# Kernel optimization log

Measured on AMD Instinct MI355X. Metric: run time of the kernel, lower is better.

## Reference

```python
import jax, jax.numpy as jnp
import numpy as np

N_NODES = 100000


def gcn_conv(x, edge_index, W, b, num_nodes):
    """PyG-style GCNConv: add self-loops, symmetric deg normalization,
    linear transform, scatter-add aggregation, bias."""
    src, dst = edge_index[0], edge_index[1]
    loop = jnp.arange(num_nodes, dtype=src.dtype)
    src = jnp.concatenate([src, loop])
    dst = jnp.concatenate([dst, loop])
    # degree (in-degree incl. self loops) and D^{-1/2}
    deg = jax.ops.segment_sum(jnp.ones_like(dst, dtype=x.dtype), dst,
                              num_segments=num_nodes)
    dinv = jnp.where(deg > 0, jax.lax.rsqrt(deg), 0.0)
    norm = dinv[src] * dinv[dst]                       # [E + N]
    h = x @ W                                          # [N, out]
    msg = h[src] * norm[:, None]                       # gather + scale
    out = jax.ops.segment_sum(msg, dst, num_segments=num_nodes)
    return out + b


def setup_inputs() -> dict:
    key = jax.random.key(0)
    ks = jax.random.split(key, 8)
    num_inputs, hidden, num_outputs = 128, 128, 2
    x = jax.random.normal(ks[0], (N_NODES, num_inputs), dtype=jnp.float32)
    edge_index = jax.random.randint(ks[1], (2, 3200000), 0, N_NODES,
                                    dtype=jnp.int64)
    s = 1.0 / np.sqrt(num_inputs)
    W1 = jax.random.uniform(ks[2], (num_inputs, hidden), jnp.float32, -s, s)
    b1 = jnp.zeros((hidden,), jnp.float32)
    s2 = 1.0 / np.sqrt(hidden)
    W2 = jax.random.uniform(ks[3], (hidden, hidden), jnp.float32, -s2, s2)
    b2 = jnp.zeros((hidden,), jnp.float32)
    Wl = jax.random.uniform(ks[4], (hidden, num_outputs), jnp.float32, -s2, s2)
    bl = jax.random.uniform(ks[5], (num_outputs,), jnp.float32, -s2, s2)
    return {"x": x, "edge_index": edge_index, "W1": W1, "b1": b1,
            "W2": W2, "b2": b2, "Wl": Wl, "bl": bl}


def reference(x, edge_index, W1, b1, W2, b2, Wl, bl):
    # eval mode: dropout is identity
    h = gcn_conv(x, edge_index, W1, b1, N_NODES)
    h = jax.nn.relu(h)
    h = gcn_conv(h, edge_index, W2, b2, N_NODES)
    h = jax.nn.relu(h)
    return h @ Wl + bl
```

## Files before the change

### kernel.cpp

```cpp
#include <hip/hip_runtime.h>
#include <hip/hip_bf16.h>


#define NB_T   256
#define NBUCK  256
#define BSHIFT 9
#define EPB    4096

__device__ __forceinline__ unsigned short f2bf(float f) {
    unsigned u = __float_as_uint(f);
    u += 0x7FFF + ((u >> 16) & 1);
    return (unsigned short)(u >> 16);
}
__device__ __forceinline__ float bflo(unsigned u) {
    return __uint_as_float(u << 16);
}
__device__ __forceinline__ float bfhi(unsigned u) {
    return __uint_as_float(u & 0xffff0000u);
}

__global__ void k_zero_buckets(int* bucketTotal) {
    bucketTotal[threadIdx.x] = 0;
}

__global__ __launch_bounds__(NB_T) void k_binCount(const int* __restrict__ src,
                                                   const int* __restrict__ dst,
                                                   int E, int n, int* bucketTotal) {
    __shared__ int hist[NBUCK];
    int t = threadIdx.x;
    hist[t] = 0;
    __syncthreads();
    int lo = blockIdx.x * EPB;
    int hi = min(lo + EPB, E + n);
    for (int e = lo + t; e < hi; e += NB_T) {
        int d = (e < E) ? dst[e] : (e - E);
        atomicAdd(&hist[d >> BSHIFT], 1);
    }
    __syncthreads();
    int h = hist[t];
    if (h) atomicAdd(&bucketTotal[t], h);
}

__global__ void k_bscan(const int* __restrict__ bucketTotal, int* bucketBase,
                        int* bucketCursor, int* rowStart, int E, int n) {
    __shared__ int sh[NBUCK];
    int t = threadIdx.x;
    int v = bucketTotal[t];
    sh[t] = v; __syncthreads();
    for (int off = 1; off < NBUCK; off <<= 1) {
        int u = (t >= off) ? sh[t - off] : 0;
        __syncthreads();
        sh[t] += u;
        __syncthreads();
    }
    int ex = sh[t] - v;
    bucketBase[t] = ex;
    bucketCursor[t] = ex;
    if (t == NBUCK - 1) { bucketBase[NBUCK] = sh[t]; rowStart[n] = E + n; }
}

__global__ __launch_bounds__(NB_T) void k_binScatter(const int* __restrict__ src,
                                                     const int* __restrict__ dst,
                                                     int E, int n, int* bucketCursor,
                                                     unsigned int* __restrict__ binned) {
    __shared__ int hist[NBUCK];
    __shared__ int base[NBUCK];
    int t = threadIdx.x;
    hist[t] = 0;
    __syncthreads();
    int lo = blockIdx.x * EPB;
    int hi = min(lo + EPB, E + n);
    for (int e = lo + t; e < hi; e += NB_T) {
        int d = (e < E) ? dst[e] : (e - E);
        atomicAdd(&hist[d >> BSHIFT], 1);
    }
    __syncthreads();
    int h = hist[t];
    if (h) base[t] = atomicAdd(&bucketCursor[t], h);
    hist[t] = 0;
    __syncthreads();
    for (int e = lo + t; e < hi; e += NB_T) {
        int s, d;
        if (e < E) { s = src[e]; d = dst[e]; }
        else       { s = d = e - E; }
        int b = d >> BSHIFT;
        int pos = base[b] + atomicAdd(&hist[b], 1);
        binned[pos] = ((unsigned)(d & 511) << 17) | (unsigned)s;
    }
}

__global__ __launch_bounds__(NB_T) void k_csr(const unsigned int* __restrict__ binned,
                                              const int* __restrict__ bucketBase,
                                              int* __restrict__ rowStart,
                                              float* __restrict__ dinv,
                                              int* __restrict__ sortedSrc, int n) {
    __shared__ int cnt[512];
    __shared__ int start[512];
    __shared__ int sh[NB_T];
    int b = blockIdx.x, t = threadIdx.x;
    int ebase = bucketBase[b], eend = bucketBase[b + 1];
    cnt[t] = 0; cnt[t + 256] = 0;
    __syncthreads();
    for (int e = ebase + t; e < eend; e += NB_T)
        atomicAdd(&cnt[binned[e] >> 17], 1);
    __syncthreads();
    int c0 = cnt[t * 2], c1 = cnt[t * 2 + 1];
    int ts = c0 + c1;
    sh[t] = ts; __syncthreads();
    for (int off = 1; off < NB_T; off <<= 1) {
        int u = (t >= off) ? sh[t - off] : 0;
        __syncthreads();
        sh[t] += u;
        __syncthreads();
    }
    int pref = sh[t] - ts;
    start[t * 2]     = pref;
    start[t * 2 + 1] = pref + c0;
    __syncthreads();
    int node0 = b << BSHIFT;
    for (int i = t; i < 512; i += NB_T) {
        int node = node0 + i;
        if (node < n) {
            rowStart[node] = ebase + start[i];
            dinv[node] = rsqrtf((float)cnt[i]);
        }
    }
    __syncthreads();
    cnt[t] = 0; cnt[t + 256] = 0;
    __syncthreads();
    for (int e = ebase + t; e < eend; e += NB_T) {
        unsigned p = binned[e];
        int i = p >> 17;
        int pos = ebase + start[i] + atomicAdd(&cnt[i], 1);
        sortedSrc[pos] = (int)(p & 0x1FFFF);
    }
}

__global__ __launch_bounds__(NB_T) void k_cvt(const float* __restrict__ x,
                                              const float* __restrict__ dinv,
                                              unsigned short* __restrict__ xh, int n) {
    int i = blockIdx.x * NB_T + threadIdx.x;
    if (i >= n * 32) return;
    float w = dinv[i >> 5];
    float4 v = *(const float4*)(x + (size_t)i * 4);
    ushort4 o;
    o.x = f2bf(v.x * w); o.y = f2bf(v.y * w);
    o.z = f2bf(v.z * w); o.w = f2bf(v.w * w);
    *(ushort4*)(xh + (size_t)i * 4) = o;
}

__global__ __launch_bounds__(256) void k_agg(const unsigned short* __restrict__ F,
                                             unsigned short* __restrict__ G,
                                             const int* __restrict__ rowStart,
                                             const int* __restrict__ sortedSrc,
                                             const float* __restrict__ dinv, int n) {
    int wave = threadIdx.x >> 6;
    int lane = threadIdx.x & 63;
    int node = blockIdx.x * 4 + wave;
    if (node >= n) return;
    int r0 = rowStart[node], r1 = rowStart[node + 1];
    int half = lane >> 5;
    int c    = lane & 31;
    size_t fo = (size_t)(c * 4);
    float a0 = 0.f, a1 = 0.f, a2 = 0.f, a3 = 0.f;
    int e = r0;
    for (; e + 8 <= r1; e += 8) {
        int s0 = sortedSrc[e     + half];
        int s1 = sortedSrc[e + 2 + half];
        int s2 = sortedSrc[e + 4 + half];
        int s3 = sortedSrc[e + 6 + half];
        uint2 v0 = *(const uint2*)(F + (size_t)s0 * 128 + fo);
        uint2 v1 = *(const uint2*)(F + (size_t)s1 * 128 + fo);
        uint2 v2 = *(const uint2*)(F + (size_t)s2 * 128 + fo);
        uint2 v3 = *(const uint2*)(F + (size_t)s3 * 128 + fo);
        a0 += bflo(v0.x) + bflo(v1.x) + bflo(v2.x) + bflo(v3.x);
        a1 += bfhi(v0.x) + bfhi(v1.x) + bfhi(v2.x) + bfhi(v3.x);
        a2 += bflo(v0.y) + bflo(v1.y) + bflo(v2.y) + bflo(v3.y);
        a3 += bfhi(v0.y) + bfhi(v1.y) + bfhi(v2.y) + bfhi(v3.y);
    }
    for (; e + 2 <= r1; e += 2) {
        int s0 = sortedSrc[e + half];
        uint2 v0 = *(const uint2*)(F + (size_t)s0 * 128 + fo);
        a0 += bflo(v0.x); a1 += bfhi(v0.x);
        a2 += bflo(v0.y); a3 += bfhi(v0.y);
    }
    if (e < r1 && half == 0) {
        int s0 = sortedSrc[e];
        uint2 v0 = *(const uint2*)(F + (size_t)s0 * 128 + fo);
        a0 += bflo(v0.x); a1 += bfhi(v0.x);
        a2 += bflo(v0.y); a3 += bfhi(v0.y);
    }
    a0 += __shfl_xor(a0, 32, 64);
    a1 += __shfl_xor(a1, 32, 64);
    a2 += __shfl_xor(a2, 32, 64);
    a3 += __shfl_xor(a3, 32, 64);
    if (half == 0) {
        float wd = dinv[node];
        ushort4 o;
        o.x = f2bf(a0 * wd); o.y = f2bf(a1 * wd);
        o.z = f2bf(a2 * wd); o.w = f2bf(a3 * wd);
        *(ushort4*)(G + (size_t)node * 128 + fo) = o;
    }
}

__device__ __forceinline__ float f4c(const float4 v, int k) {
    return k == 0 ? v.x : k == 1 ? v.y : k == 2 ? v.z : v.w;
}

template <bool BF16OUT>
__global__ __launch_bounds__(256, 4) void k_gemm(const unsigned short* __restrict__ F,
                                                 const float* __restrict__ W,
                                                 const float* __restrict__ bias,
                                                 void* __restrict__ Gout,
                                                 const float* __restrict__ dinv, int n) {
    __shared__ float x_lds[64 * 132];
    int t = threadIdx.x;
    int tileBase = blockIdx.x * 64;

    #pragma unroll
    for (int i = 0; i < 4; i++) {
        int idx = i * 256 + t;
        int row = idx >> 4;
        int c8  = (idx & 15) * 8;
        int grow = tileBase + row;
        uint4 v = make_uint4(0, 0, 0, 0);
        if (grow < n) v = *(const uint4*)(F + (size_t)grow * 128 + c8);
        float* dst = &x_lds[row * 132 + c8];
        dst[0] = bflo(v.x); dst[1] = bfhi(v.x);
        dst[2] = bflo(v.y); dst[3] = bfhi(v.y);
        dst[4] = bflo(v.z); dst[5] = bfhi(v.z);
        dst[6] = bflo(v.w); dst[7] = bfhi(v.w);
    }
    __syncthreads();

    int r0 = (t >> 4) * 4;
    int c0 = (t & 15) * 4;
    float acc[4][8];
    #pragma unroll
    for (int i = 0; i < 4; i++)
        #pragma unroll
        for (int j = 0; j < 8; j++) acc[i][j] = 0.f;

    for (int k0 = 0; k0 < 128; k0 += 4) {
        float4 xv[4];
        #pragma unroll
        for (int i = 0; i < 4; i++) xv[i] = *(float4*)&x_lds[(r0 + i) * 132 + k0];
        #pragma unroll
        for (int kk = 0; kk < 4; kk++) {
            float4 w1 = *(const float4*)&W[(k0 + kk) * 128 + c0];
            float4 w2 = *(const float4*)&W[(k0 + kk) * 128 + c0 + 64];
            #pragma unroll
            for (int i = 0; i < 4; i++) {
                float xs = f4c(xv[i], kk);
                acc[i][0] += xs * w1.x; acc[i][1] += xs * w1.y;
                acc[i][2] += xs * w1.z; acc[i][3] += xs * w1.w;
                acc[i][4] += xs * w2.x; acc[i][5] += xs * w2.y;
                acc[i][6] += xs * w2.z; acc[i][7] += xs * w2.w;
            }
        }
    }

    float bv[8];
    #pragma unroll
    for (int j = 0; j < 4; j++) { bv[j] = bias[c0 + j]; bv[4 + j] = bias[c0 + 64 + j]; }
    #pragma unroll
    for (int i = 0; i < 4; i++) {
        int grow = tileBase + r0 + i;
        if (grow < n) {
            float r[8];
            #pragma unroll
            for (int j = 0; j < 8; j++) r[j] = fmaxf(acc[i][j] + bv[j], 0.f);
            if (BF16OUT) {
                float w = dinv[grow];
                ushort4 o1, o2;
                o1.x = f2bf(r[0] * w); o1.y = f2bf(r[1] * w);
                o1.z = f2bf(r[2] * w); o1.w = f2bf(r[3] * w);
                o2.x = f2bf(r[4] * w); o2.y = f2bf(r[5] * w);
                o2.z = f2bf(r[6] * w); o2.w = f2bf(r[7] * w);
                unsigned short* G = (unsigned short*)Gout;
                *(ushort4*)&G[(size_t)grow * 128 + c0]      = o1;
                *(ushort4*)&G[(size_t)grow * 128 + c0 + 64] = o2;
            } else {
                float* G = (float*)Gout;
                *(float4*)&G[(size_t)grow * 128 + c0]      = make_float4(r[0], r[1], r[2], r[3]);
                *(float4*)&G[(size_t)grow * 128 + c0 + 64] = make_float4(r[4], r[5], r[6], r[7]);
            }
        }
    }
}

__global__ __launch_bounds__(256) void k_out(const float* __restrict__ F,
                                             const float* __restrict__ Wl,
                                             const float* __restrict__ bl,
                                             float* __restrict__ out, int n) {
    int wave = threadIdx.x >> 6;
    int lane = threadIdx.x & 63;
    int node = blockIdx.x * 4 + wave;
    if (node >= n) return;
    int f = lane * 2;
    float2 v = *(const float2*)(F + (size_t)node * 128 + f);
    float w00 = Wl[f * 2 + 0], w01 = Wl[f * 2 + 1];
    float w10 = Wl[f * 2 + 2], w11 = Wl[f * 2 + 3];
    float a0 = v.x * w00 + v.y * w10;
    float a1 = v.x * w01 + v.y * w11;
    for (int m = 32; m >= 1; m >>= 1) {
        a0 += __shfl_xor(a0, m, 64);
        a1 += __shfl_xor(a1, m, 64);
    }
    if (lane == 0) {
        out[(size_t)node * 2 + 0] = a0 + bl[0];
        out[(size_t)node * 2 + 1] = a1 + bl[1];
    }
}

extern "C" void kernel_launch(void* const* d_in, const int* in_sizes, int n_in,
                              void* d_out, int out_size, void* d_ws, size_t ws_size,
                              hipStream_t stream) {
    const float* x   = (const float*)d_in[0];
    const int*   ei  = (const int*)d_in[1];
    const float* W1  = (const float*)d_in[2];
    const float* b1  = (const float*)d_in[3];
    const float* W2  = (const float*)d_in[4];
    const float* b2  = (const float*)d_in[5];
    const float* Wl  = (const float*)d_in[6];
    const float* bl  = (const float*)d_in[7];
    float*       out = (float*)d_out;

    const int N = in_sizes[0] / 128;
    const int E = in_sizes[1] / 2;
    const int* src = ei;
    const int* dst = ei + E;

    char* p = (char*)d_ws;
    auto alloc = [&](size_t bytes) -> char* {
        char* r = p;
        p += (bytes + 511) & ~(size_t)511;
        return r;
    };
    float* dinv         = (float*)alloc((size_t)N * 4);
    int*   rowStart     = (int*)alloc((size_t)(N + 1) * 4);
    int*   bucketTotal  = (int*)alloc(NBUCK * 4);
    int*   bucketBase   = (int*)alloc((NBUCK + 1) * 4);
    int*   bucketCursor = (int*)alloc(NBUCK * 4);
    int*   sortedSrc    = (int*)alloc((size_t)(E + N) * 4);
    float* A            = (float*)alloc((size_t)N * 128 * 4);
    float* B            = (float*)alloc((size_t)N * 128 * 4);
    unsigned int*   binned = (unsigned int*)A;
    unsigned short* Abf    = (unsigned short*)A;
    unsigned short* xh     = (unsigned short*)B;

    int nbBin  = (E + N + EPB - 1) / EPB;
    int nBuckA = (N + 511) >> BSHIFT;

    k_zero_buckets<<<1, NBUCK, 0, stream>>>(bucketTotal);
    k_binCount<<<nbBin, NB_T, 0, stream>>>(src, dst, E, N, bucketTotal);
    k_bscan<<<1, NBUCK, 0, stream>>>(bucketTotal, bucketBase, bucketCursor, rowStart, E, N);
    k_binScatter<<<nbBin, NB_T, 0, stream>>>(src, dst, E, N, bucketCursor, binned);
    k_csr<<<nBuckA, NB_T, 0, stream>>>(binned, bucketBase, rowStart, dinv, sortedSrc, N);

    k_cvt<<<(N * 32 + NB_T - 1) / NB_T, NB_T, 0, stream>>>(x, dinv, xh, N);
    k_agg<<<(N + 3) / 4, NB_T, 0, stream>>>(xh, Abf, rowStart, sortedSrc, dinv, N);
    k_gemm<true><<<(N + 63) / 64, NB_T, 0, stream>>>(Abf, W1, b1, (void*)xh, dinv, N);
    k_agg<<<(N + 3) / 4, NB_T, 0, stream>>>(xh, Abf, rowStart, sortedSrc, dinv, N);
    k_gemm<false><<<(N + 63) / 64, NB_T, 0, stream>>>(Abf, W2, b2, (void*)B, dinv, N);
    k_out<<<(N + 3) / 4, NB_T, 0, stream>>>(B, Wl, bl, out, N);
}
```

Before: 584.6 us.

## Use bf16 MFMA for dense GCN layer GEMMs with pretransposed bf16 weights

Replaces the FP32 scalar-FMA tiled GEMM with a wave-level bf16 MFMA 16x16x32 GEMM. A-fragments are read directly from the bf16 aggregated features, and the weights are staged in LDS. A new kernel converts and transposes each weight matrix to bf16 before use. This aims to cut the ALU cost of the linear transforms, in exchange for weights rounded to bf16 and scalar, less vectorized output stores.

```diff
diff --git a/kernel.cpp b/kernel.cpp
--- a/kernel.cpp
+++ b/kernel.cpp
@@ -6,6 +6,9 @@
 #define NBUCK  256
 #define BSHIFT 9
 #define EPB    4096
+
+typedef __attribute__((ext_vector_type(8))) short bf16x8;
+typedef __attribute__((ext_vector_type(4))) float f32x4;
 
 __device__ __forceinline__ unsigned short f2bf(float f) {
     unsigned u = __float_as_uint(f);
@@ -147,6 +150,13 @@
     o.x = f2bf(v.x * w); o.y = f2bf(v.y * w);
     o.z = f2bf(v.z * w); o.w = f2bf(v.w * w);
     *(ushort4*)(xh + (size_t)i * 4) = o;
+}
+
+__global__ __launch_bounds__(NB_T) void k_cvtW(const float* __restrict__ W,
+                                               unsigned short* __restrict__ Wt) {
+    int i = blockIdx.x * NB_T + threadIdx.x;
+    int c = i >> 7, k = i & 127;
+    Wt[c * 128 + k] = f2bf(W[k * 128 + c]);
 }
 
 __global__ __launch_bounds__(256) void k_agg(const unsigned short* __restrict__ F,
@@ -203,87 +213,63 @@
     }
 }
 
-__device__ __forceinline__ float f4c(const float4 v, int k) {
-    return k == 0 ? v.x : k == 1 ? v.y : k == 2 ? v.z : v.w;
-}
-
 template <bool BF16OUT>
 __global__ __launch_bounds__(256, 4) void k_gemm(const unsigned short* __restrict__ F,
-                                                 const float* __restrict__ W,
+                                                 const unsigned short* __restrict__ Wt,
                                                  const float* __restrict__ bias,
                                                  void* __restrict__ Gout,
                                                  const float* __restrict__ dinv, int n) {
-    __shared__ float x_lds[64 * 132];
+    __shared__ unsigned short wlds[128][136];
     int t = threadIdx.x;
-    int tileBase = blockIdx.x * 64;
-
-    #pragma unroll
-    for (int i = 0; i < 4; i++) {
+
+    #pragma unroll
+    for (int i = 0; i < 8; i++) {
         int idx = i * 256 + t;
-        int row = idx >> 4;
-        int c8  = (idx & 15) * 8;
-        int grow = tileBase + row;
-        uint4 v = make_uint4(0, 0, 0, 0);
-        if (grow < n) v = *(const uint4*)(F + (size_t)grow * 128 + c8);
-        float* dst = &x_lds[row * 132 + c8];
-        dst[0] = bflo(v.x); dst[1] = bfhi(v.x);
-        dst[2] = bflo(v.y); dst[3] = bfhi(v.y);
-        dst[4] = bflo(v.z); dst[5] = bfhi(v.z);
-        dst[6] = bflo(v.w); dst[7] = bfhi(v.w);
-    }
-    __syncthreads();
-
-    int r0 = (t >> 4) * 4;
-    int c0 = (t & 15) * 4;
-    float acc[4][8];
-    #pragma unroll
-    for (int i = 0; i < 4; i++)
-        #pragma unroll
-        for (int j = 0; j < 8; j++) acc[i][j] = 0.f;
-
-    for (int k0 = 0; k0 < 128; k0 += 4) {
-        float4 xv[4];
-        #pragma unroll
-        for (int i = 0; i < 4; i++) xv[i] = *(float4*)&x_lds[(r0 + i) * 132 + k0];
+        int col = idx >> 4, seg = idx & 15;
+        uint4 v = *(const uint4*)(Wt + col * 128 + seg * 8);
+        *(uint4*)&wlds[col][seg * 8] = v;
+    }
+    __syncthreads();
+
+    int wv = t >> 6, l = t & 63;
+    int rl = l & 15;
+    int kg = l >> 4;
+    int rowA = blockIdx.x * 64 + wv * 16 + rl;
+
+    bf16x8 afr[4];
+    #pragma unroll
+    for (int kk = 0; kk < 4; kk++) {
+        if (rowA < n) afr[kk] = *(const bf16x8*)(F + (size_t)rowA * 128 + kk * 32 + kg * 8);
+        else          afr[kk] = (bf16x8)(short)0;
+    }
+
+    f32x4 acc[8];
+    #pragma unroll
+    for (int c16 = 0; c16 < 8; c16++) acc[c16] = (f32x4)0.f;
+
+    #pragma unroll
+    for (int c16 = 0; c16 < 8; c16++) {
         #pragma unroll
         for (int kk = 0; kk < 4; kk++) {
-            float4 w1 = *(const float4*)&W[(k0 + kk) * 128 + c0];
-            float4 w2 = *(const float4*)&W[(k0 + kk) * 128 + c0 + 64];
-            #pragma unroll
-            for (int i = 0; i < 4; i++) {
-                float xs = f4c(xv[i], kk);
-                acc[i][0] += xs * w1.x; acc[i][1] += xs * w1.y;
-                acc[i][2] += xs * w1.z; acc[i][3] += xs * w1.w;
-                acc[i][4] += xs * w2.x; acc[i][5] += xs * w2.y;
-                acc[i][6] += xs * w2.z; acc[i][7] += xs * w2.w;
-            }
+            bf16x8 bfr = *(const bf16x8*)&wlds[c16 * 16 + rl][kk * 32 + kg * 8];
+            acc[c16] = __builtin_amdgcn_mfma_f32_16x16x32_bf16(afr[kk], bfr, acc[c16], 0, 0, 0);
         }
     }
 
-    float bv[8];
-    #pragma unroll
-    for (int j = 0; j < 4; j++) { bv[j] = bias[c0 + j]; bv[4 + j] = bias[c0 + 64 + j]; }
-    #pragma unroll
-    for (int i = 0; i < 4; i++) {
-        int grow = tileBase + r0 + i;
-        if (grow < n) {
-            float r[8];
-            #pragma unroll
-            for (int j = 0; j < 8; j++) r[j] = fmaxf(acc[i][j] + bv[j], 0.f);
+    int rowBase = blockIdx.x * 64 + wv * 16 + kg * 4;
+    #pragma unroll
+    for (int r = 0; r < 4; r++) {
+        int rowo = rowBase + r;
+        if (rowo >= n) continue;
+        float w = BF16OUT ? dinv[rowo] : 1.f;
+        #pragma unroll
+        for (int c16 = 0; c16 < 8; c16++) {
+            int col = c16 * 16 + rl;
+            float v = fmaxf(acc[c16][r] + bias[col], 0.f);
             if (BF16OUT) {
-                float w = dinv[grow];
-                ushort4 o1, o2;
-                o1.x = f2bf(r[0] * w); o1.y = f2bf(r[1] * w);
-                o1.z = f2bf(r[2] * w); o1.w = f2bf(r[3] * w);
-                o2.x = f2bf(r[4] * w); o2.y = f2bf(r[5] * w);
-                o2.z = f2bf(r[6] * w); o2.w = f2bf(r[7] * w);
-                unsigned short* G = (unsigned short*)Gout;
-                *(ushort4*)&G[(size_t)grow * 128 + c0]      = o1;
-                *(ushort4*)&G[(size_t)grow * 128 + c0 + 64] = o2;
+                ((unsigned short*)Gout)[(size_t)rowo * 128 + col] = f2bf(v * w);
             } else {
-                float* G = (float*)Gout;
-                *(float4*)&G[(size_t)grow * 128 + c0]      = make_float4(r[0], r[1], r[2], r[3]);
-                *(float4*)&G[(size_t)grow * 128 + c0 + 64] = make_float4(r[4], r[5], r[6], r[7]);
+                ((float*)Gout)[(size_t)rowo * 128 + col] = v;
             }
         }
     }
@@ -343,6 +329,8 @@
     int*   bucketBase   = (int*)alloc((NBUCK + 1) * 4);
     int*   bucketCursor = (int*)alloc(NBUCK * 4);
     int*   sortedSrc    = (int*)alloc((size_t)(E + N) * 4);
+    unsigned short* Wt1 = (unsigned short*)alloc(128 * 128 * 2);
+    unsigned short* Wt2 = (unsigned short*)alloc(128 * 128 * 2);
     float* A            = (float*)alloc((size_t)N * 128 * 4);
     float* B            = (float*)alloc((size_t)N * 128 * 4);
     unsigned int*   binned = (unsigned int*)A;
@@ -357,11 +345,13 @@
     k_bscan<<<1, NBUCK, 0, stream>>>(bucketTotal, bucketBase, bucketCursor, rowStart, E, N);
     k_binScatter<<<nbBin, NB_T, 0, stream>>>(src, dst, E, N, bucketCursor, binned);
     k_csr<<<nBuckA, NB_T, 0, stream>>>(binned, bucketBase, rowStart, dinv, sortedSrc, N);
+    k_cvtW<<<64, NB_T, 0, stream>>>(W1, Wt1);
+    k_cvtW<<<64, NB_T, 0, stream>>>(W2, Wt2);
 
     k_cvt<<<(N * 32 + NB_T - 1) / NB_T, NB_T, 0, stream>>>(x, dinv, xh, N);
     k_agg<<<(N + 3) / 4, NB_T, 0, stream>>>(xh, Abf, rowStart, sortedSrc, dinv, N);
-    k_gemm<true><<<(N + 63) / 64, NB_T, 0, stream>>>(Abf, W1, b1, (void*)xh, dinv, N);
+    k_gemm<true><<<(N + 63) / 64, NB_T, 0, stream>>>(Abf, Wt1, b1, (void*)xh, dinv, N);
     k_agg<<<(N + 3) / 4, NB_T, 0, stream>>>(xh, Abf, rowStart, sortedSrc, dinv, N);
-    k_gemm<false><<<(N + 63) / 64, NB_T, 0, stream>>>(Abf, W2, b2, (void*)B, dinv, N);
+    k_gemm<false><<<(N + 63) / 64, NB_T, 0, stream>>>(Abf, Wt2, b2, (void*)B, dinv, N);
     k_out<<<(N + 3) / 4, NB_T, 0, stream>>>(B, Wl, bl, out, N);
 }
```

Result: faster. 497.5 us (-14.9%).
